# Performance work log

Hardware: AMD Instinct MI355X
Metric: run time of the kernel (lower is better)

Reference implementation:

```python
import jax, jax.numpy as jnp
import numpy as np

HIDDEN = 1024
INTER = 4096
NUM_EXPERTS = 8
TOP_K = 2


def setup_inputs() -> dict:
    key = jax.random.key(0)
    k1, k2, k3, k4 = jax.random.split(key, 4)
    hidden_states = jax.random.normal(k1, (4, 1024, HIDDEN), dtype=jnp.float32)
    gate_w = jax.random.normal(k2, (HIDDEN, NUM_EXPERTS), dtype=jnp.float32) * 0.02
    w1 = jax.random.normal(k3, (NUM_EXPERTS, HIDDEN, INTER), dtype=jnp.float32) * 0.02
    w2 = jax.random.normal(k4, (NUM_EXPERTS, INTER, HIDDEN), dtype=jnp.float32) * 0.02
    return {"hidden_states": hidden_states, "gate_w": gate_w, "w1": w1, "w2": w2}


def reference(hidden_states, gate_w, w1, w2):
    B, S, H = hidden_states.shape
    x = hidden_states.reshape(-1, H)                       # [T, H]
    T = x.shape[0]
    router_logits = x @ gate_w                             # [T, E]
    probs = jax.nn.softmax(router_logits.astype(jnp.float32), axis=-1)
    routing_weights, selected_experts = jax.lax.top_k(probs, TOP_K)  # [T, K]
    routing_weights = routing_weights / routing_weights.sum(-1, keepdims=True)
    routing_weights = routing_weights.astype(x.dtype)
    # combine[t, e] = sum_k rw[t, k] * (sel[t, k] == e)
    combine = jnp.zeros((T, NUM_EXPERTS), x.dtype).at[
        jnp.arange(T)[:, None], selected_experts
    ].add(routing_weights)
    # dense grouped MLP over all experts; zero combine weight drops unrouted pairs
    h1 = jax.nn.gelu(jnp.einsum('th,ehi->tei', x, w1), approximate=False)  # [T, E, I]
    y = jnp.einsum('tei,eih->teh', h1, w2)                 # [T, E, H]
    out = jnp.einsum('teh,te->th', y, combine)             # [T, H]
    return out.reshape(B, S, H), router_logits
```

## Files before the change

### kernel.cpp

```cpp
#include <hip/hip_runtime.h>
#include <hip/hip_bf16.h>
#include <math.h>

typedef unsigned short u16;
typedef unsigned int u32;
typedef __bf16 bf16x8 __attribute__((ext_vector_type(8)));
typedef float f32x4 __attribute__((ext_vector_type(4)));

#define T_TOK 4096
#define HID   1024
#define INTER 4096
#define NEXP  8

#define WS_NEEDED 209978368ull

__device__ __forceinline__ u16 f2bf(float f) {
    u32 u = __builtin_bit_cast(u32, f);
    u += 0x7FFFu + ((u >> 16) & 1u);
    return (u16)(u >> 16);
}

__device__ __forceinline__ void gl2lds16(const void* g, void* l) {
    __builtin_amdgcn_global_load_lds(
        (const __attribute__((address_space(1))) u32*)g,
        (__attribute__((address_space(3))) u32*)l, 16, 0, 0);
}

__device__ __forceinline__ float fast_gelu(float v) {
    float u2 = v * (-1.5957691216f - 0.0713548163f * v * v);
    return v / (1.0f + __expf(u2));
}

__global__ __launch_bounds__(256) void router_kernel(
    const float* __restrict__ x, const float* __restrict__ gw,
    float* __restrict__ logits, int* __restrict__ counts,
    int* __restrict__ tlist, float* __restrict__ wlist)
{
    const int lane = threadIdx.x & 63, wv = threadIdx.x >> 6;
    const int t = blockIdx.x * 4 + wv;
    const float* xr = x + (size_t)t * HID;
    float a[8] = {0.f,0.f,0.f,0.f,0.f,0.f,0.f,0.f};
    for (int h = lane; h < HID; h += 64) {
        float xv = xr[h];
        const float4* g4 = (const float4*)(gw + h * 8);
        float4 g0 = g4[0], g1 = g4[1];
        a[0] += xv * g0.x; a[1] += xv * g0.y; a[2] += xv * g0.z; a[3] += xv * g0.w;
        a[4] += xv * g1.x; a[5] += xv * g1.y; a[6] += xv * g1.z; a[7] += xv * g1.w;
    }
#pragma unroll
    for (int e = 0; e < 8; e++) {
        float v = a[e];
        for (int o = 32; o > 0; o >>= 1) v += __shfl_down(v, o, 64);
        a[e] = v;
    }
    if (lane == 0) {
#pragma unroll
        for (int e = 0; e < 8; e++) logits[(size_t)t * 8 + e] = a[e];
        int e1 = 0; float b1 = a[0];
        for (int e = 1; e < 8; e++) if (a[e] > b1) { b1 = a[e]; e1 = e; }
        int e2 = -1; float b2 = -1e30f;
        for (int e = 0; e < 8; e++) if (e != e1 && a[e] > b2) { b2 = a[e]; e2 = e; }
        float wa = 1.0f / (1.0f + expf(b2 - b1));
        float wb = 1.0f - wa;
        int p = atomicAdd(&counts[e1], 1);
        tlist[e1 * T_TOK + p] = t; wlist[e1 * T_TOK + p] = wa;
        p = atomicAdd(&counts[e2], 1);
        tlist[e2 * T_TOK + p] = t; wlist[e2 * T_TOK + p] = wb;
    }
}

__global__ void scan_kernel(const int* __restrict__ counts, int* __restrict__ offs)
{
    if (threadIdx.x == 0) {
        int s = 0;
        for (int e = 0; e < 8; e++) { offs[e] = s; s += counts[e]; }
    }
}

__global__ __launch_bounds__(256) void convert_x_kernel(
    const float* __restrict__ src, u16* __restrict__ dst)
{
    const int idx = (blockIdx.x * 256 + threadIdx.x) * 8;
    float4 f0 = *(const float4*)(src + idx);
    float4 f1 = *(const float4*)(src + idx + 4);
    uint4 o;
    o.x = (u32)f2bf(f0.x) | ((u32)f2bf(f0.y) << 16);
    o.y = (u32)f2bf(f0.z) | ((u32)f2bf(f0.w) << 16);
    o.z = (u32)f2bf(f1.x) | ((u32)f2bf(f1.y) << 16);
    o.w = (u32)f2bf(f1.z) | ((u32)f2bf(f1.w) << 16);
    *(uint4*)(dst + idx) = o;
}

__global__ __launch_bounds__(256) void transpose_convert_kernel(
    const float* __restrict__ src, u16* __restrict__ dst, int R, int C)
{
    __shared__ float tl[64][65];
    const int e = blockIdx.z;
    const int c0 = blockIdx.x * 64, r0 = blockIdx.y * 64;
    const float* s = src + (size_t)e * R * C + (size_t)r0 * C + c0;
    const int tid = threadIdx.x;
#pragma unroll
    for (int it = 0; it < 4; it++) {
        int idx = it * 256 + tid;
        int r = idx >> 4;
        int c4 = (idx & 15) * 4;
        float4 v = *(const float4*)(s + (size_t)r * C + c4);
        tl[c4 + 0][r] = v.x;
        tl[c4 + 1][r] = v.y;
        tl[c4 + 2][r] = v.z;
        tl[c4 + 3][r] = v.w;
    }
    __syncthreads();
    u16* d = dst + (size_t)e * C * R + (size_t)c0 * R + r0;
#pragma unroll
    for (int it = 0; it < 2; it++) {
        int idx = it * 256 + tid;
        int c = idx >> 3;
        int rg = (idx & 7) * 8;
        u32 o[4];
#pragma unroll
        for (int p = 0; p < 4; p++)
            o[p] = (u32)f2bf(tl[c][rg + 2 * p]) | ((u32)f2bf(tl[c][rg + 2 * p + 1]) << 16);
        *(uint4*)(d + (size_t)c * R + rg) = *(uint4*)o;
    }
}

__global__ __launch_bounds__(256, 1) void gemm1_kernel(
    const u16* __restrict__ xb, const u16* __restrict__ w1t,
    const int* __restrict__ counts, const int* __restrict__ offs,
    const int* __restrict__ tlist, u16* __restrict__ h1b)
{
    const int e = blockIdx.z, mt = blockIdx.y, nt = blockIdx.x;
    const int cnt = counts[e];
    if (mt * 128 >= cnt) return;
    __shared__ __align__(16) u16 As[8192];
    __shared__ __align__(16) u16 Bs[8192];
    __shared__ int toks[128];
    const int tid = threadIdx.x, lane = tid & 63, wv = tid >> 6;
    if (tid < 128) toks[tid] = tlist[e * T_TOK + min(mt * 128 + tid, cnt - 1)];
    __syncthreads();

    f32x4 acc[4][4] = {};
    const int wm = wv & 1, wn = wv >> 1;
    const int sj = tid >> 3, sp = tid & 7;

    size_t abase[4], bbase[4];
    const u16* w1base = w1t + ((size_t)e * INTER + (size_t)nt * 128) * HID;
#pragma unroll
    for (int j = 0; j < 4; j++) {
        int m = j * 32 + sj;
        abase[j] = (size_t)toks[m] * HID + ((sp - m) & 7) * 8;
        bbase[j] = (size_t)m * HID + ((sp - m) & 7) * 8;
    }

    for (int h0 = 0; h0 < HID; h0 += 64) {
#pragma unroll
        for (int j = 0; j < 4; j++)
            gl2lds16(xb + abase[j] + h0, &As[j * 2048 + wv * 512]);
#pragma unroll
        for (int j = 0; j < 4; j++)
            gl2lds16(w1base + bbase[j] + h0, &Bs[j * 2048 + wv * 512]);
        __syncthreads();
#pragma unroll
        for (int kk = 0; kk < 2; kk++) {
            bf16x8 a[4], b[4];
            const int jjb = kk * 4 + (lane >> 4);
#pragma unroll
            for (int i = 0; i < 4; i++) {
                int m = wm * 64 + i * 16 + (lane & 15);
                a[i] = *(const bf16x8*)&As[m * 64 + ((jjb + m) & 7) * 8];
            }
#pragma unroll
            for (int i = 0; i < 4; i++) {
                int n = wn * 64 + i * 16 + (lane & 15);
                b[i] = *(const bf16x8*)&Bs[n * 64 + ((jjb + n) & 7) * 8];
            }
#pragma unroll
            for (int i = 0; i < 4; i++)
#pragma unroll
                for (int j = 0; j < 4; j++)
                    acc[i][j] = __builtin_amdgcn_mfma_f32_16x16x32_bf16(
                        a[i], b[j], acc[i][j], 0, 0, 0);
        }
        __syncthreads();
    }

    const int pb = offs[e] + mt * 128;
    const bool full = (mt * 128 + 128 <= cnt);
#pragma unroll
    for (int i = 0; i < 4; i++) {
        const int mb = wm * 64 + i * 16 + ((lane >> 4) << 2);
#pragma unroll
        for (int j = 0; j < 4; j++) {
            const int n = nt * 128 + wn * 64 + j * 16 + (lane & 15);
#pragma unroll
            for (int r = 0; r < 4; r++) {
                const int m = mb + r;
                if (full || mt * 128 + m < cnt) {
                    h1b[(size_t)(pb + m) * INTER + n] = f2bf(fast_gelu(acc[i][j][r]));
                }
            }
        }
    }
}

__global__ __launch_bounds__(256, 1) void gemm2_kernel(
    const u16* __restrict__ h1b, const u16* __restrict__ w2t,
    const int* __restrict__ counts, const int* __restrict__ offs,
    const int* __restrict__ tlist, const float* __restrict__ wlist,
    float* __restrict__ out)
{
    const int e = blockIdx.z, mt = blockIdx.y;
    const int nt = blockIdx.x & 7, ks = blockIdx.x >> 3;
    const int cnt = counts[e];
    if (mt * 128 >= cnt) return;
    __shared__ __align__(16) u16 As[8192];
    __shared__ __align__(16) u16 Bs[8192];
    __shared__ int toks[128];
    __shared__ float wgt[128];
    const int tid = threadIdx.x, lane = tid & 63, wv = tid >> 6;
    if (tid < 128) {
        int gi = e * T_TOK + min(mt * 128 + tid, cnt - 1);
        toks[tid] = tlist[gi];
        wgt[tid] = wlist[gi];
    }
    __syncthreads();

    f32x4 acc[4][4] = {};
    const int wm = wv & 1, wn = wv >> 1;
    const int sj = tid >> 3, sp = tid & 7;

    size_t abase[4], bbase[4];
    const u16* w2base = w2t + ((size_t)e * HID + (size_t)nt * 128) * INTER;
    const int prow = offs[e];
#pragma unroll
    for (int j = 0; j < 4; j++) {
        int m = j * 32 + sj;
        int row = prow + min(mt * 128 + m, cnt - 1);
        abase[j] = (size_t)row * INTER + ((sp - m) & 7) * 8;
        bbase[j] = (size_t)m * INTER + ((sp - m) & 7) * 8;
    }

    const int i_lo = ks * (INTER / 2), i_hi = i_lo + (INTER / 2);
    for (int i0 = i_lo; i0 < i_hi; i0 += 64) {
#pragma unroll
        for (int j = 0; j < 4; j++)
            gl2lds16(h1b + abase[j] + i0, &As[j * 2048 + wv * 512]);
#pragma unroll
        for (int j = 0; j < 4; j++)
            gl2lds16(w2base + bbase[j] + i0, &Bs[j * 2048 + wv * 512]);
        __syncthreads();
#pragma unroll
        for (int kk = 0; kk < 2; kk++) {
            bf16x8 a[4], b[4];
            const int jjb = kk * 4 + (lane >> 4);
#pragma unroll
            for (int i = 0; i < 4; i++) {
                int m = wm * 64 + i * 16 + (lane & 15);
                a[i] = *(const bf16x8*)&As[m * 64 + ((jjb + m) & 7) * 8];
            }
#pragma unroll
            for (int i = 0; i < 4; i++) {
                int n = wn * 64 + i * 16 + (lane & 15);
                b[i] = *(const bf16x8*)&Bs[n * 64 + ((jjb + n) & 7) * 8];
            }
#pragma unroll
            for (int i = 0; i < 4; i++)
#pragma unroll
                for (int j = 0; j < 4; j++)
                    acc[i][j] = __builtin_amdgcn_mfma_f32_16x16x32_bf16(
                        a[i], b[j], acc[i][j], 0, 0, 0);
        }
        __syncthreads();
    }

    const bool full = (mt * 128 + 128 <= cnt);
#pragma unroll
    for (int i = 0; i < 4; i++) {
        const int mb = wm * 64 + i * 16 + ((lane >> 4) << 2);
#pragma unroll
        for (int j = 0; j < 4; j++) {
            const int n = nt * 128 + wn * 64 + j * 16 + (lane & 15);
#pragma unroll
            for (int r = 0; r < 4; r++) {
                const int m = mb + r;
                if (full || mt * 128 + m < cnt) {
                    atomicAdd(&out[(size_t)toks[m] * HID + n], acc[i][j][r] * wgt[m]);
                }
            }
        }
    }
}

extern "C" void kernel_launch(void* const* d_in, const int* in_sizes, int n_in,
                              void* d_out, int out_size, void* d_ws, size_t ws_size,
                              hipStream_t stream)
{
    const float* x  = (const float*)d_in[0];
    const float* gw = (const float*)d_in[1];
    const float* w1 = (const float*)d_in[2];
    const float* w2 = (const float*)d_in[3];
    float* out    = (float*)d_out;
    float* logits = out + 4194304;

    char* ws = (char*)d_ws;
    int*   counts = (int*)ws;
    int*   offs   = (int*)(ws + 256);
    int*   tlist  = (int*)(ws + 1024);
    float* wlist  = (float*)(ws + 132096);
    u16*   xb     = (u16*)(ws + 263168);
    u16*   w1t    = (u16*)(ws + 8651776);
    u16*   w2t    = (u16*)(ws + 75760640);
    u16*   h1b    = (u16*)(ws + 142869504);

    if (ws_size < WS_NEEDED) return;

    hipMemsetAsync(out, 0, 4194304 * sizeof(float), stream);
    hipMemsetAsync(counts, 0, 256, stream);

    router_kernel<<<1024, 256, 0, stream>>>(x, gw, logits, counts, tlist, wlist);
    scan_kernel<<<1, 64, 0, stream>>>(counts, offs);
    convert_x_kernel<<<2048, 256, 0, stream>>>(x, xb);
    transpose_convert_kernel<<<dim3(64, 16, 8), 256, 0, stream>>>(w1, w1t, HID, INTER);
    transpose_convert_kernel<<<dim3(16, 64, 8), 256, 0, stream>>>(w2, w2t, INTER, HID);

    gemm1_kernel<<<dim3(32, 16, 8), 256, 0, stream>>>(xb, w1t, counts, offs, tlist, h1b);
    gemm2_kernel<<<dim3(16, 16, 8), 256, 0, stream>>>(h1b, w2t, counts, offs, tlist, wlist, out);
}
```

Measured before the change: 707.5 us.

## Fuse x conversion into router, coarsen transposes, interleave expert block order, split-K 4

The bf16 conversion of x moves into the router kernel, removing one launch and a second read of x. The weight transpose kernels now process four 64-row tiles per block, giving fewer blocks with more work each. The GEMM grids become 1D with the expert index in the low bits, so blocks from different experts interleave and load stays balanced across CUs. gemm2 splits K four ways instead of two, which adds parallelism but doubles the atomic adds into the output.

```diff
diff --git a/kernel.cpp b/kernel.cpp
--- a/kernel.cpp
+++ b/kernel.cpp
@@ -12,6 +12,10 @@
 #define INTER 4096
 #define NEXP  8
 
+#define BM 128
+#define BN 128
+#define BK 64
+
 #define WS_NEEDED 209978368ull
 
 __device__ __forceinline__ u16 f2bf(float f) {
@@ -34,7 +38,8 @@
 __global__ __launch_bounds__(256) void router_kernel(
     const float* __restrict__ x, const float* __restrict__ gw,
     float* __restrict__ logits, int* __restrict__ counts,
-    int* __restrict__ tlist, float* __restrict__ wlist)
+    int* __restrict__ tlist, float* __restrict__ wlist,
+    u16* __restrict__ xb)
 {
     const int lane = threadIdx.x & 63, wv = threadIdx.x >> 6;
     const int t = blockIdx.x * 4 + wv;
@@ -46,6 +51,18 @@
         float4 g0 = g4[0], g1 = g4[1];
         a[0] += xv * g0.x; a[1] += xv * g0.y; a[2] += xv * g0.z; a[3] += xv * g0.w;
         a[4] += xv * g1.x; a[5] += xv * g1.y; a[6] += xv * g1.z; a[7] += xv * g1.w;
+    }
+#pragma unroll
+    for (int seg = 0; seg < 2; seg++) {
+        int h = seg * 512 + lane * 8;
+        float4 f0 = *(const float4*)(xr + h);
+        float4 f1 = *(const float4*)(xr + h + 4);
+        uint4 o;
+        o.x = (u32)f2bf(f0.x) | ((u32)f2bf(f0.y) << 16);
+        o.y = (u32)f2bf(f0.z) | ((u32)f2bf(f0.w) << 16);
+        o.z = (u32)f2bf(f1.x) | ((u32)f2bf(f1.y) << 16);
+        o.w = (u32)f2bf(f1.z) | ((u32)f2bf(f1.w) << 16);
+        *(uint4*)(xb + (size_t)t * HID + h) = o;
     }
 #pragma unroll
     for (int e = 0; e < 8; e++) {
@@ -77,51 +94,45 @@
     }
 }
 
-__global__ __launch_bounds__(256) void convert_x_kernel(
-    const float* __restrict__ src, u16* __restrict__ dst)
-{
-    const int idx = (blockIdx.x * 256 + threadIdx.x) * 8;
-    float4 f0 = *(const float4*)(src + idx);
-    float4 f1 = *(const float4*)(src + idx + 4);
-    uint4 o;
-    o.x = (u32)f2bf(f0.x) | ((u32)f2bf(f0.y) << 16);
-    o.y = (u32)f2bf(f0.z) | ((u32)f2bf(f0.w) << 16);
-    o.z = (u32)f2bf(f1.x) | ((u32)f2bf(f1.y) << 16);
-    o.w = (u32)f2bf(f1.z) | ((u32)f2bf(f1.w) << 16);
-    *(uint4*)(dst + idx) = o;
-}
-
-__global__ __launch_bounds__(256) void transpose_convert_kernel(
+template<int TAG>
+__global__ __launch_bounds__(256) void transpose_convert(
     const float* __restrict__ src, u16* __restrict__ dst, int R, int C)
 {
     __shared__ float tl[64][65];
     const int e = blockIdx.z;
-    const int c0 = blockIdx.x * 64, r0 = blockIdx.y * 64;
-    const float* s = src + (size_t)e * R * C + (size_t)r0 * C + c0;
+    const int c0 = blockIdx.x * 64;
     const int tid = threadIdx.x;
-#pragma unroll
-    for (int it = 0; it < 4; it++) {
-        int idx = it * 256 + tid;
-        int r = idx >> 4;
-        int c4 = (idx & 15) * 4;
-        float4 v = *(const float4*)(s + (size_t)r * C + c4);
-        tl[c4 + 0][r] = v.x;
-        tl[c4 + 1][r] = v.y;
-        tl[c4 + 2][r] = v.z;
-        tl[c4 + 3][r] = v.w;
-    }
-    __syncthreads();
-    u16* d = dst + (size_t)e * C * R + (size_t)c0 * R + r0;
-#pragma unroll
-    for (int it = 0; it < 2; it++) {
-        int idx = it * 256 + tid;
-        int c = idx >> 3;
-        int rg = (idx & 7) * 8;
-        u32 o[4];
-#pragma unroll
-        for (int p = 0; p < 4; p++)
-            o[p] = (u32)f2bf(tl[c][rg + 2 * p]) | ((u32)f2bf(tl[c][rg + 2 * p + 1]) << 16);
-        *(uint4*)(d + (size_t)c * R + rg) = *(uint4*)o;
+    const float* sbase = src + (size_t)e * R * C + c0;
+    u16* dbase = dst + (size_t)e * C * R + (size_t)c0 * R;
+#pragma unroll
+    for (int sub = 0; sub < 4; sub++) {
+        const int r0 = (blockIdx.y * 4 + sub) * 64;
+        const float* s = sbase + (size_t)r0 * C;
+#pragma unroll
+        for (int it = 0; it < 4; it++) {
+            int idx = it * 256 + tid;
+            int r = idx >> 4;
+            int c4 = (idx & 15) * 4;
+            float4 v = *(const float4*)(s + (size_t)r * C + c4);
+            tl[c4 + 0][r] = v.x;
+            tl[c4 + 1][r] = v.y;
+            tl[c4 + 2][r] = v.z;
+            tl[c4 + 3][r] = v.w;
+        }
+        __syncthreads();
+        u16* d = dbase + r0;
+#pragma unroll
+        for (int it = 0; it < 2; it++) {
+            int idx = it * 256 + tid;
+            int c = idx >> 3;
+            int rg = (idx & 7) * 8;
+            u32 o[4];
+#pragma unroll
+            for (int p = 0; p < 4; p++)
+                o[p] = (u32)f2bf(tl[c][rg + 2 * p]) | ((u32)f2bf(tl[c][rg + 2 * p + 1]) << 16);
+            *(uint4*)(d + (size_t)c * R + rg) = *(uint4*)o;
+        }
+        __syncthreads();
     }
 }
 
@@ -130,14 +141,17 @@
     const int* __restrict__ counts, const int* __restrict__ offs,
     const int* __restrict__ tlist, u16* __restrict__ h1b)
 {
-    const int e = blockIdx.z, mt = blockIdx.y, nt = blockIdx.x;
+    const int g = blockIdx.x & 7, p = blockIdx.x >> 3;
+    const int e = g;
+    const int nt = p >> 4;
+    const int mt = p & 15;
     const int cnt = counts[e];
-    if (mt * 128 >= cnt) return;
-    __shared__ __align__(16) u16 As[8192];
-    __shared__ __align__(16) u16 Bs[8192];
-    __shared__ int toks[128];
+    if (mt * BM >= cnt) return;
+    __shared__ __align__(16) u16 As[BM * BK];
+    __shared__ __align__(16) u16 Bs[BN * BK];
+    __shared__ int toks[BM];
     const int tid = threadIdx.x, lane = tid & 63, wv = tid >> 6;
-    if (tid < 128) toks[tid] = tlist[e * T_TOK + min(mt * 128 + tid, cnt - 1)];
+    if (tid < BM) toks[tid] = tlist[e * T_TOK + min(mt * BM + tid, cnt - 1)];
     __syncthreads();
 
     f32x4 acc[4][4] = {};
@@ -145,7 +159,7 @@
     const int sj = tid >> 3, sp = tid & 7;
 
     size_t abase[4], bbase[4];
-    const u16* w1base = w1t + ((size_t)e * INTER + (size_t)nt * 128) * HID;
+    const u16* w1base = w1t + ((size_t)e * INTER + (size_t)nt * BN) * HID;
 #pragma unroll
     for (int j = 0; j < 4; j++) {
         int m = j * 32 + sj;
@@ -153,7 +167,7 @@
         bbase[j] = (size_t)m * HID + ((sp - m) & 7) * 8;
     }
 
-    for (int h0 = 0; h0 < HID; h0 += 64) {
+    for (int h0 = 0; h0 < HID; h0 += BK) {
 #pragma unroll
         for (int j = 0; j < 4; j++)
             gl2lds16(xb + abase[j] + h0, &As[j * 2048 + wv * 512]);
@@ -185,20 +199,19 @@
         __syncthreads();
     }
 
-    const int pb = offs[e] + mt * 128;
-    const bool full = (mt * 128 + 128 <= cnt);
+    const int pb = offs[e] + mt * BM;
+    const bool full = (mt * BM + BM <= cnt);
 #pragma unroll
     for (int i = 0; i < 4; i++) {
         const int mb = wm * 64 + i * 16 + ((lane >> 4) << 2);
 #pragma unroll
         for (int j = 0; j < 4; j++) {
-            const int n = nt * 128 + wn * 64 + j * 16 + (lane & 15);
+            const int n = nt * BN + wn * 64 + j * 16 + (lane & 15);
 #pragma unroll
             for (int r = 0; r < 4; r++) {
                 const int m = mb + r;
-                if (full || mt * 128 + m < cnt) {
+                if (full || mt * BM + m < cnt)
                     h1b[(size_t)(pb + m) * INTER + n] = f2bf(fast_gelu(acc[i][j][r]));
-                }
             }
         }
     }
@@ -210,17 +223,20 @@
     const int* __restrict__ tlist, const float* __restrict__ wlist,
     float* __restrict__ out)
 {
-    const int e = blockIdx.z, mt = blockIdx.y;
-    const int nt = blockIdx.x & 7, ks = blockIdx.x >> 3;
+    const int g = blockIdx.x & 7, p = blockIdx.x >> 3;
+    const int e = g;
+    const int ks = (p >> 7) & 3;
+    const int nt = (p >> 4) & 7;
+    const int mt = p & 15;
     const int cnt = counts[e];
-    if (mt * 128 >= cnt) return;
-    __shared__ __align__(16) u16 As[8192];
-    __shared__ __align__(16) u16 Bs[8192];
-    __shared__ int toks[128];
-    __shared__ float wgt[128];
+    if (mt * BM >= cnt) return;
+    __shared__ __align__(16) u16 As[BM * BK];
+    __shared__ __align__(16) u16 Bs[BN * BK];
+    __shared__ int toks[BM];
+    __shared__ float wgt[BM];
     const int tid = threadIdx.x, lane = tid & 63, wv = tid >> 6;
-    if (tid < 128) {
-        int gi = e * T_TOK + min(mt * 128 + tid, cnt - 1);
+    if (tid < BM) {
+        int gi = e * T_TOK + min(mt * BM + tid, cnt - 1);
         toks[tid] = tlist[gi];
         wgt[tid] = wlist[gi];
     }
@@ -231,18 +247,18 @@
     const int sj = tid >> 3, sp = tid & 7;
 
     size_t abase[4], bbase[4];
-    const u16* w2base = w2t + ((size_t)e * HID + (size_t)nt * 128) * INTER;
+    const u16* w2base = w2t + ((size_t)e * HID + (size_t)nt * BN) * INTER;
     const int prow = offs[e];
 #pragma unroll
     for (int j = 0; j < 4; j++) {
         int m = j * 32 + sj;
-        int row = prow + min(mt * 128 + m, cnt - 1);
+        int row = prow + min(mt * BM + m, cnt - 1);
         abase[j] = (size_t)row * INTER + ((sp - m) & 7) * 8;
         bbase[j] = (size_t)m * INTER + ((sp - m) & 7) * 8;
     }
 
-    const int i_lo = ks * (INTER / 2), i_hi = i_lo + (INTER / 2);
-    for (int i0 = i_lo; i0 < i_hi; i0 += 64) {
+    const int i_lo = ks * (INTER / 4), i_hi = i_lo + (INTER / 4);
+    for (int i0 = i_lo; i0 < i_hi; i0 += BK) {
 #pragma unroll
         for (int j = 0; j < 4; j++)
             gl2lds16(h1b + abase[j] + i0, &As[j * 2048 + wv * 512]);
@@ -274,19 +290,18 @@
         __syncthreads();
     }
 
-    const bool full = (mt * 128 + 128 <= cnt);
+    const bool full = (mt * BM + BM <= cnt);
 #pragma unroll
     for (int i = 0; i < 4; i++) {
         const int mb = wm * 64 + i * 16 + ((lane >> 4) << 2);
 #pragma unroll
         for (int j = 0; j < 4; j++) {
-            const int n = nt * 128 + wn * 64 + j * 16 + (lane & 15);
+            const int n = nt * BN + wn * 64 + j * 16 + (lane & 15);
 #pragma unroll
             for (int r = 0; r < 4; r++) {
                 const int m = mb + r;
-                if (full || mt * 128 + m < cnt) {
+                if (full || mt * BM + m < cnt)
                     atomicAdd(&out[(size_t)toks[m] * HID + n], acc[i][j][r] * wgt[m]);
-                }
             }
         }
     }
@@ -318,12 +333,11 @@
     hipMemsetAsync(out, 0, 4194304 * sizeof(float), stream);
     hipMemsetAsync(counts, 0, 256, stream);
 
-    router_kernel<<<1024, 256, 0, stream>>>(x, gw, logits, counts, tlist, wlist);
+    router_kernel<<<1024, 256, 0, stream>>>(x, gw, logits, counts, tlist, wlist, xb);
     scan_kernel<<<1, 64, 0, stream>>>(counts, offs);
-    convert_x_kernel<<<2048, 256, 0, stream>>>(x, xb);
-    transpose_convert_kernel<<<dim3(64, 16, 8), 256, 0, stream>>>(w1, w1t, HID, INTER);
-    transpose_convert_kernel<<<dim3(16, 64, 8), 256, 0, stream>>>(w2, w2t, INTER, HID);
-
-    gemm1_kernel<<<dim3(32, 16, 8), 256, 0, stream>>>(xb, w1t, counts, offs, tlist, h1b);
-    gemm2_kernel<<<dim3(16, 16, 8), 256, 0, stream>>>(h1b, w2t, counts, offs, tlist, wlist, out);
-}
+    transpose_convert<1><<<dim3(64, 4, 8), 256, 0, stream>>>(w1, w1t, HID, INTER);
+    transpose_convert<2><<<dim3(16, 16, 8), 256, 0, stream>>>(w2, w2t, INTER, HID);
+
+    gemm1_kernel<<<4096, 256, 0, stream>>>(xb, w1t, counts, offs, tlist, h1b);
+    gemm2_kernel<<<4096, 256, 0, stream>>>(h1b, w2t, counts, offs, tlist, wlist, out);
+}
```

After: 779.4 us. 1.1x slower.
